# Kernel optimization log

Measured on AMD Instinct MI355X. Metric: run time of the kernel, lower is better.

The kernel has to match this reference:

```python
import jax, jax.numpy as jnp
import numpy as np

DIM = 2048
N_HEADS = 16
N_KV_HEADS = 4
HEAD_DIM = 128
SLIDING_WINDOW = 1024
ROPE_BASE = 10000.0


def _rotate_half(x):
    d = x.shape[-1] // 2
    return jnp.concatenate((-x[..., d:], x[..., :d]), axis=-1)


def _rope_cos_sin(T, dtype):
    inv_freq = 1.0 / (ROPE_BASE ** (jnp.arange(0, HEAD_DIM, 2, dtype=jnp.float32) / HEAD_DIM))
    t = jnp.arange(T, dtype=jnp.float32)
    freqs = jnp.outer(t, inv_freq)            # [T, HEAD_DIM//2]
    emb = jnp.concatenate((freqs, freqs), axis=-1)  # [T, HEAD_DIM]
    return jnp.cos(emb).astype(dtype), jnp.sin(emb).astype(dtype)


def setup_inputs() -> dict:
    key = jax.random.key(0)
    kx, kq, kk, kv, ko = jax.random.split(key, 5)
    s_in = 1.0 / np.sqrt(DIM)
    s_o = 1.0 / np.sqrt(N_HEADS * HEAD_DIM)
    return {
        "x": jax.random.normal(kx, (1, 4096, DIM), dtype=jnp.float32),
        "Wq": jax.random.normal(kq, (DIM, N_HEADS * HEAD_DIM), dtype=jnp.float32) * s_in,
        "Wk": jax.random.normal(kk, (DIM, N_KV_HEADS * HEAD_DIM), dtype=jnp.float32) * s_in,
        "Wv": jax.random.normal(kv, (DIM, N_KV_HEADS * HEAD_DIM), dtype=jnp.float32) * s_in,
        "Wo": jax.random.normal(ko, (N_HEADS * HEAD_DIM, DIM), dtype=jnp.float32) * s_o,
    }


def reference(x, Wq, Wk, Wv, Wo):
    B, T, C = x.shape
    # projections -> [B, H, T, D]
    q = (x @ Wq).reshape(B, T, N_HEADS, HEAD_DIM).transpose(0, 2, 1, 3)
    k = (x @ Wk).reshape(B, T, N_KV_HEADS, HEAD_DIM).transpose(0, 2, 1, 3)
    v = (x @ Wv).reshape(B, T, N_KV_HEADS, HEAD_DIM).transpose(0, 2, 1, 3)

    cos, sin = _rope_cos_sin(T, x.dtype)      # [T, D], broadcast over B, H
    q = q * cos + _rotate_half(q) * sin
    k = k * cos + _rotate_half(k) * sin

    # GQA: repeat kv heads (repeat_interleave over head axis)
    kv_rep = N_HEADS // N_KV_HEADS
    k = jnp.repeat(k, kv_rep, axis=1)
    v = jnp.repeat(v, kv_rep, axis=1)

    scale = 1.0 / np.sqrt(HEAD_DIM)
    att = jnp.einsum("bhqd,bhkd->bhqk", q, k) * scale  # [B, H, T, T]

    i = jnp.arange(T)[:, None]
    j = jnp.arange(T)[None, :]
    allowed = (j <= i) & ((i - j) < SLIDING_WINDOW)     # causal + sliding window
    att = jnp.where(allowed, att, -jnp.inf)
    att = jax.nn.softmax(att, axis=-1)

    y = jnp.einsum("bhqk,bhkd->bhqd", att, v)           # [B, H, T, D]
    y = y.transpose(0, 2, 1, 3).reshape(B, T, N_HEADS * HEAD_DIM)
    return y @ Wo
```

## Files before the change

kernel.cpp:

```cpp
#include <hip/hip_runtime.h>
#include <math.h>

typedef __bf16 bf16;
typedef __bf16 bf16x8 __attribute__((ext_vector_type(8)));
typedef __bf16 bf16x4 __attribute__((ext_vector_type(4)));
typedef float f32x4 __attribute__((ext_vector_type(4)));

__device__ __forceinline__ void ldg_lds16(const bf16* g, bf16* l) {
#if __has_builtin(__builtin_amdgcn_global_load_lds)
    __builtin_amdgcn_global_load_lds(
        (const __attribute__((address_space(1))) void*)g,
        (__attribute__((address_space(3))) void*)l, 16, 0, 0);
#else
    *(bf16x8*)l = *(const bf16x8*)g;
#endif
}

__global__ void cvt_x(const float* __restrict__ X, bf16* __restrict__ Xb, int total8)
{
    int idx = blockIdx.x * 256 + threadIdx.x;
    if (idx >= total8) return;
    const float* p = X + (size_t)idx * 8;
    f32x4 a = *reinterpret_cast<const f32x4*>(p);
    f32x4 b = *reinterpret_cast<const f32x4*>(p + 4);
    bf16x8 r;
    r[0] = (bf16)a[0]; r[1] = (bf16)a[1]; r[2] = (bf16)a[2]; r[3] = (bf16)a[3];
    r[4] = (bf16)b[0]; r[5] = (bf16)b[1]; r[6] = (bf16)b[2]; r[7] = (bf16)b[3];
    *reinterpret_cast<bf16x8*>(Xb + (size_t)idx * 8) = r;
}

__global__ void cvt_wt3(const float* __restrict__ Wq, const float* __restrict__ Wk,
                        const float* __restrict__ Wv, bf16* __restrict__ Wt)
{
    __shared__ float t[32][33];
    int bx = blockIdx.x;
    const float* W; int Ncols, nbase;
    if (bx < 64)      { W = Wq; Ncols = 2048; nbase = 0;    }
    else if (bx < 80) { W = Wk; Ncols = 512;  nbase = 2048; bx -= 64; }
    else              { W = Wv; Ncols = 512;  nbase = 2560; bx -= 80; }
    const int n0 = bx * 32, k0 = blockIdx.y * 32;
    const int x = threadIdx.x, y = threadIdx.y;
    #pragma unroll
    for (int i = 0; i < 4; ++i)
        t[y + 8 * i][x] = W[(size_t)(k0 + y + 8 * i) * Ncols + n0 + x];
    __syncthreads();
    #pragma unroll
    for (int i = 0; i < 4; ++i)
        Wt[(size_t)(nbase + n0 + y + 8 * i) * 2048 + k0 + x] = (bf16)t[x][y + 8 * i];
}

__global__ void cvt_wt(const float* __restrict__ W, bf16* __restrict__ Wt, int Ncols)
{
    __shared__ float t[32][33];
    const int n0 = blockIdx.x * 32, k0 = blockIdx.y * 32;
    const int x = threadIdx.x, y = threadIdx.y;
    #pragma unroll
    for (int i = 0; i < 4; ++i)
        t[y + 8 * i][x] = W[(size_t)(k0 + y + 8 * i) * Ncols + n0 + x];
    __syncthreads();
    #pragma unroll
    for (int i = 0; i < 4; ++i)
        Wt[(size_t)(n0 + y + 8 * i) * 2048 + k0 + x] = (bf16)t[x][y + 8 * i];
}

__global__ __launch_bounds__(512, 2) void gemm256_qkv(
    const bf16* __restrict__ A, const bf16* __restrict__ Bt,
    bf16* __restrict__ Qo, bf16* __restrict__ Ko, bf16* __restrict__ Vt,
    int K)
{
    __shared__ __align__(16) bf16 smem[2 * 32768];

    const int tid  = threadIdx.x;
    const int lane = tid & 63;
    const int wave = tid >> 6;
    const int quad = lane >> 4;
    const int l16  = lane & 15;
    const int wm   = wave >> 2;
    const int wn   = wave & 3;

    const int m0 = blockIdx.y * 256;
    const int n0 = blockIdx.x * 256;

    int offA[4], offB[4];
    #pragma unroll
    for (int p = 0; p < 4; ++p) {
        int u = p * 512 + tid;
        int row = u >> 3;
        int kc8 = (u & 7) ^ (row & 7);
        offA[p] = (m0 + row) * K + kc8 * 8;
        offB[p] = (n0 + row) * K + kc8 * 8;
    }
    const int dstoff = tid * 8;

    const int xv = (l16 & 7) << 4;
    const int c0 = ((quad * 16) ^ xv) >> 1;
    const int c1 = ((64 + quad * 16) ^ xv) >> 1;
    const int rA = (wm * 128 + l16) * 64;
    const int rB = (wn * 64 + l16) * 64;

    f32x4 acc[8][4] = {};
    const int NT = K >> 6;

    {
        bf16* d0 = smem;
        bf16* d1 = smem + 32768;
        #pragma unroll
        for (int p = 0; p < 4; ++p) {
            ldg_lds16(A  + offA[p], d0 + p * 4096 + dstoff);
            ldg_lds16(Bt + offB[p], d0 + 16384 + p * 4096 + dstoff);
        }
        #pragma unroll
        for (int p = 0; p < 4; ++p) {
            ldg_lds16(A  + offA[p] + 64, d1 + p * 4096 + dstoff);
            ldg_lds16(Bt + offB[p] + 64, d1 + 16384 + p * 4096 + dstoff);
        }
    }
    asm volatile("s_waitcnt vmcnt(8)" ::: "memory");
    __builtin_amdgcn_sched_barrier(0);
    __builtin_amdgcn_s_barrier();
    __builtin_amdgcn_sched_barrier(0);

    for (int t = 0; t < NT; ++t) {
        const bf16* As = smem + (t & 1) * 32768;
        const bf16* Bs = As + 16384;

        bf16x8 a0[8], b0[4];
        #pragma unroll
        for (int i = 0; i < 8; ++i)
            a0[i] = *(const bf16x8*)(As + rA + i * 1024 + c0);
        #pragma unroll
        for (int i = 0; i < 4; ++i)
            b0[i] = *(const bf16x8*)(Bs + rB + i * 1024 + c0);

        #pragma unroll
        for (int mi = 0; mi < 8; ++mi)
            #pragma unroll
            for (int ni = 0; ni < 4; ++ni)
                acc[mi][ni] = __builtin_amdgcn_mfma_f32_16x16x32_bf16(
                    a0[mi], b0[ni], acc[mi][ni], 0, 0, 0);

        bf16x8 a1[8], b1[4];
        #pragma unroll
        for (int i = 0; i < 8; ++i)
            a1[i] = *(const bf16x8*)(As + rA + i * 1024 + c1);
        #pragma unroll
        for (int i = 0; i < 4; ++i)
            b1[i] = *(const bf16x8*)(Bs + rB + i * 1024 + c1);

        asm volatile("s_waitcnt lgkmcnt(0)" ::: "memory");
        __builtin_amdgcn_sched_barrier(0);
        __builtin_amdgcn_s_barrier();
        __builtin_amdgcn_sched_barrier(0);

        if (t + 2 < NT) {
            bf16* d = smem + (t & 1) * 32768;
            const int koff = (t + 2) * 64;
            #pragma unroll
            for (int p = 0; p < 4; ++p) {
                ldg_lds16(A  + offA[p] + koff, d + p * 4096 + dstoff);
                ldg_lds16(Bt + offB[p] + koff, d + 16384 + p * 4096 + dstoff);
            }
        }

        __builtin_amdgcn_s_setprio(1);
        #pragma unroll
        for (int mi = 0; mi < 8; ++mi)
            #pragma unroll
            for (int ni = 0; ni < 4; ++ni)
                acc[mi][ni] = __builtin_amdgcn_mfma_f32_16x16x32_bf16(
                    a1[mi], b1[ni], acc[mi][ni], 0, 0, 0);
        __builtin_amdgcn_s_setprio(0);

        if (t + 2 < NT) {
            asm volatile("s_waitcnt vmcnt(8)" ::: "memory");
            __builtin_amdgcn_sched_barrier(0);
            __builtin_amdgcn_s_barrier();
            __builtin_amdgcn_sched_barrier(0);
        } else if (t == NT - 2) {
            asm volatile("s_waitcnt vmcnt(0)" ::: "memory");
            __builtin_amdgcn_sched_barrier(0);
            __builtin_amdgcn_s_barrier();
            __builtin_amdgcn_sched_barrier(0);
        }
    }

    #pragma unroll
    for (int mi = 0; mi < 8; ++mi) {
        #pragma unroll
        for (int ni = 0; ni < 4; ++ni) {
            const int row = m0 + wm * 128 + mi * 16 + quad * 4;
            const int col = n0 + wn * 64 + ni * 16 + l16;
            if (n0 < 2048) {
                #pragma unroll
                for (int r = 0; r < 4; ++r)
                    Qo[(size_t)(row + r) * 2048 + col] = (bf16)acc[mi][ni][r];
            } else if (n0 < 2560) {
                #pragma unroll
                for (int r = 0; r < 4; ++r)
                    Ko[(size_t)(row + r) * 512 + (col - 2048)] = (bf16)acc[mi][ni][r];
            } else {
                bf16x4 v;
                #pragma unroll
                for (int r = 0; r < 4; ++r) v[r] = (bf16)acc[mi][ni][r];
                *reinterpret_cast<bf16x4*>(&Vt[(size_t)(col - 2560) * 4096 + row]) = v;
            }
        }
    }
}

__global__ __launch_bounds__(512, 2) void gemm_out(
    const bf16* __restrict__ A, const bf16* __restrict__ Bt,
    float* __restrict__ C, int K)
{
    __shared__ __align__(16) bf16 smem[2 * 24576];

    const int tid  = threadIdx.x;
    const int lane = tid & 63;
    const int wave = tid >> 6;
    const int quad = lane >> 4;
    const int l16  = lane & 15;
    const int wm   = wave >> 1;
    const int wn   = wave & 1;

    const int m0 = blockIdx.y * 256;
    const int n0 = blockIdx.x * 128;

    int offA[4], offB[2];
    #pragma unroll
    for (int p = 0; p < 4; ++p) {
        int u = p * 512 + tid;
        int row = u >> 3;
        int kc8 = (u & 7) ^ (row & 7);
        offA[p] = (m0 + row) * K + kc8 * 8;
    }
    #pragma unroll
    for (int p = 0; p < 2; ++p) {
        int u = p * 512 + tid;
        int row = u >> 3;
        int kc8 = (u & 7) ^ (row & 7);
        offB[p] = (n0 + row) * K + kc8 * 8;
    }
    const int dstoff = tid * 8;

    const int xv = (l16 & 7) << 4;
    const int c0 = ((quad * 16) ^ xv) >> 1;
    const int c1 = ((64 + quad * 16) ^ xv) >> 1;
    const int rA = (wm * 64 + l16) * 64;
    const int rB = (wn * 64 + l16) * 64;

    f32x4 acc[4][4] = {};
    const int NT = K >> 6;

    auto stage = [&](int tt, int bsel) {
        bf16* as = smem + bsel * 24576;
        bf16* bs = as + 16384;
        const int koff = tt * 64;
        #pragma unroll
        for (int p = 0; p < 4; ++p)
            ldg_lds16(A + offA[p] + koff, as + p * 4096 + dstoff);
        #pragma unroll
        for (int p = 0; p < 2; ++p)
            ldg_lds16(Bt + offB[p] + koff, bs + p * 4096 + dstoff);
    };

    stage(0, 0);
    stage(1, 1);
    asm volatile("s_waitcnt vmcnt(6)" ::: "memory");
    __builtin_amdgcn_sched_barrier(0);
    __builtin_amdgcn_s_barrier();
    __builtin_amdgcn_sched_barrier(0);

    for (int t = 0; t < NT; ++t) {
        const bf16* As = smem + (t & 1) * 24576;
        const bf16* Bs = As + 16384;

        bf16x8 a0[4], b0[4];
        #pragma unroll
        for (int i = 0; i < 4; ++i)
            a0[i] = *(const bf16x8*)(As + rA + i * 1024 + c0);
        #pragma unroll
        for (int i = 0; i < 4; ++i)
            b0[i] = *(const bf16x8*)(Bs + rB + i * 1024 + c0);

        #pragma unroll
        for (int mi = 0; mi < 4; ++mi)
            #pragma unroll
            for (int ni = 0; ni < 4; ++ni)
                acc[mi][ni] = __builtin_amdgcn_mfma_f32_16x16x32_bf16(
                    a0[mi], b0[ni], acc[mi][ni], 0, 0, 0);

        bf16x8 a1[4], b1[4];
        #pragma unroll
        for (int i = 0; i < 4; ++i)
            a1[i] = *(const bf16x8*)(As + rA + i * 1024 + c1);
        #pragma unroll
        for (int i = 0; i < 4; ++i)
            b1[i] = *(const bf16x8*)(Bs + rB + i * 1024 + c1);

        asm volatile("s_waitcnt lgkmcnt(0)" ::: "memory");
        __builtin_amdgcn_sched_barrier(0);
        __builtin_amdgcn_s_barrier();
        __builtin_amdgcn_sched_barrier(0);

        if (t + 2 < NT) stage(t + 2, t & 1);

        __builtin_amdgcn_s_setprio(1);
        #pragma unroll
        for (int mi = 0; mi < 4; ++mi)
            #pragma unroll
            for (int ni = 0; ni < 4; ++ni)
                acc[mi][ni] = __builtin_amdgcn_mfma_f32_16x16x32_bf16(
                    a1[mi], b1[ni], acc[mi][ni], 0, 0, 0);
        __builtin_amdgcn_s_setprio(0);

        if (t + 2 < NT) {
            asm volatile("s_waitcnt vmcnt(6)" ::: "memory");
            __builtin_amdgcn_sched_barrier(0);
            __builtin_amdgcn_s_barrier();
            __builtin_amdgcn_sched_barrier(0);
        } else if (t == NT - 2) {
            asm volatile("s_waitcnt vmcnt(0)" ::: "memory");
            __builtin_amdgcn_sched_barrier(0);
            __builtin_amdgcn_s_barrier();
            __builtin_amdgcn_sched_barrier(0);
        }
    }

    #pragma unroll
    for (int mi = 0; mi < 4; ++mi) {
        #pragma unroll
        for (int ni = 0; ni < 4; ++ni) {
            const int row = m0 + wm * 64 + mi * 16 + quad * 4;
            const int col = n0 + wn * 64 + ni * 16 + l16;
            #pragma unroll
            for (int r = 0; r < 4; ++r)
                C[(size_t)(row + r) * 2048 + col] = acc[mi][ni][r];
        }
    }
}

__global__ void rope2_kernel(bf16* __restrict__ Qb, bf16* __restrict__ Kb,
                             int qtot, int ktot)
{
    int idx = blockIdx.x * 256 + threadIdx.x;
    bf16* base; int logH;
    if (idx < qtot) { base = Qb; logH = 4; }
    else {
        idx -= qtot;
        if (idx >= ktot) return;
        base = Kb; logH = 2;
    }
    int j  = idx & 63;
    int th = idx >> 6;
    int t  = th >> logH;

    bf16* p = base + (size_t)th * 128;
    const float NEG_LN1E4_64 = -0.14391155806323211f;
    float inv_freq = expf(NEG_LN1E4_64 * (float)j);
    float ang = (float)t * inv_freq;
    float c = cosf(ang), s = sinf(ang);
    float q0 = (float)p[j], q1 = (float)p[j + 64];
    p[j]      = (bf16)(q0 * c - q1 * s);
    p[j + 64] = (bf16)(q1 * c + q0 * s);
}

__global__ __launch_bounds__(256) void attn_v7(
    const bf16* __restrict__ Q, const bf16* __restrict__ K,
    const bf16* __restrict__ Vt, bf16* __restrict__ Y)
{
    const float scale = 0.08838834764831845f;

    __shared__ __align__(16) bf16 Ks[2 * 64 * 128];
    __shared__ __align__(16) bf16 Vs[2 * 128 * 64];
    __shared__ __align__(16) bf16 Pl[4][16 * 72];

    const int tid  = threadIdx.x;
    const int lane = tid & 63;
    const int wave = tid >> 6;
    const int quad = lane >> 4;
    const int l16  = lane & 15;

    const int i0  = (gridDim.x - 1 - blockIdx.x) * 64;
    const int h   = blockIdx.y;
    const int kvh = h >> 2;
    const int q0  = i0 + wave * 16;
    bf16* Plw = Pl[wave];

    bf16x8 qf[4];
    {
        const bf16* qp = Q + (size_t)(q0 + l16) * 2048 + h * 128 + quad * 8;
        #pragma unroll
        for (int c = 0; c < 4; ++c)
            qf[c] = *reinterpret_cast<const bf16x8*>(qp + c * 32);
    }

    f32x4 o[8] = {};
    float lsum[4] = {0.f, 0.f, 0.f, 0.f};

    const int ks = (i0 >= 1024) ? (i0 - 1024) : 0;
    const int nsteps = (i0 + 64 - ks) >> 6;

    auto stage = [&](int tt, int bsel) {
        const int k0s = ks + tt * 64;
        bf16* kd = Ks + bsel * 8192;
        bf16* vd = Vs + bsel * 8192;
        #pragma unroll
        for (int p = 0; p < 4; ++p) {
            int u = p * 256 + tid;
            int kk = u >> 4, sc = u & 15;
            ldg_lds16(K + (size_t)(k0s + kk) * 512 + kvh * 128 + (sc ^ (kk & 15)) * 8,
                      kd + u * 8);
        }
        #pragma unroll
        for (int p = 0; p < 4; ++p) {
            int u = p * 256 + tid;
            int d = u >> 3, sc = u & 7;
            ldg_lds16(Vt + (size_t)(kvh * 128 + d) * 4096 + k0s + (sc ^ (d & 7)) * 8,
                      vd + u * 8);
        }
    };

    stage(0, 0);
    stage(1, 1);
    asm volatile("s_waitcnt vmcnt(8)" ::: "memory");
    __builtin_amdgcn_sched_barrier(0);
    __builtin_amdgcn_s_barrier();
    __builtin_amdgcn_sched_barrier(0);

    for (int t = 0; t < nsteps; ++t) {
        const int b  = t & 1;
        const int k0 = ks + t * 64;
        const bf16* Kb = Ks + b * 8192;
        const bf16* Vb = Vs + b * 8192;

        f32x4 s[4];
        __builtin_amdgcn_s_setprio(1);
        #pragma unroll
        for (int kh = 0; kh < 4; ++kh) {
            const int kk = kh * 16 + l16;
            f32x4 sv = {};
            #pragma unroll
            for (int c = 0; c < 4; ++c) {
                bf16x8 kf = *reinterpret_cast<const bf16x8*>(
                    &Kb[kk * 128 + (((c * 4 + quad) ^ (kk & 15)) * 8)]);
                sv = __builtin_amdgcn_mfma_f32_16x16x32_bf16(qf[c], kf, sv, 0, 0, 0);
            }
            s[kh] = sv;
        }
        __builtin_amdgcn_s_setprio(0);

        #pragma unroll
        for (int kh = 0; kh < 4; ++kh) {
            const int key = k0 + kh * 16 + l16;
            #pragma unroll
            for (int r = 0; r < 4; ++r) {
                const int qrow = q0 + quad * 4 + r;
                bool ok = (unsigned)(qrow - key) < 1024u;
                float pv = ok ? __expf(s[kh][r] * scale) : 0.f;
                lsum[r] += pv;
                Plw[(quad * 4 + r) * 72 + kh * 16 + l16] = (bf16)pv;
            }
        }

        bf16x8 pf0 = *reinterpret_cast<const bf16x8*>(&Plw[l16 * 72 + quad * 8]);
        bf16x8 pf1 = *reinterpret_cast<const bf16x8*>(&Plw[l16 * 72 + 32 + quad * 8]);
        __builtin_amdgcn_s_setprio(1);
        #pragma unroll
        for (int n = 0; n < 8; ++n) {
            const int d = n * 16 + l16;
            bf16x8 v0 = *reinterpret_cast<const bf16x8*>(
                &Vb[d * 64 + (((quad) ^ (d & 7)) * 8)]);
            bf16x8 v1 = *reinterpret_cast<const bf16x8*>(
                &Vb[d * 64 + (((4 + quad) ^ (d & 7)) * 8)]);
            o[n] = __builtin_amdgcn_mfma_f32_16x16x32_bf16(pf0, v0, o[n], 0, 0, 0);
            o[n] = __builtin_amdgcn_mfma_f32_16x16x32_bf16(pf1, v1, o[n], 0, 0, 0);
        }
        __builtin_amdgcn_s_setprio(0);

        asm volatile("s_waitcnt lgkmcnt(0)" ::: "memory");
        __builtin_amdgcn_sched_barrier(0);
        __builtin_amdgcn_s_barrier();
        __builtin_amdgcn_sched_barrier(0);

        if (t + 2 < nsteps) {
            stage(t + 2, b);
            asm volatile("s_waitcnt vmcnt(8)" ::: "memory");
        } else {
            asm volatile("s_waitcnt vmcnt(0)" ::: "memory");
        }
        __builtin_amdgcn_sched_barrier(0);
        __builtin_amdgcn_s_barrier();
        __builtin_amdgcn_sched_barrier(0);
    }

    #pragma unroll
    for (int r = 0; r < 4; ++r) {
        #pragma unroll
        for (int off = 1; off < 16; off <<= 1)
            lsum[r] += __shfl_xor(lsum[r], off, 64);
    }
    #pragma unroll
    for (int r = 0; r < 4; ++r) {
        int row = q0 + quad * 4 + r;
        float inv = (lsum[r] > 0.f) ? 1.f / lsum[r] : 0.f;
        #pragma unroll
        for (int n = 0; n < 8; ++n)
            Y[(size_t)row * 2048 + h * 128 + n * 16 + l16] = (bf16)(o[n][r] * inv);
    }
}

extern "C" void kernel_launch(void* const* d_in, const int* in_sizes, int n_in,
                              void* d_out, int out_size, void* d_ws, size_t ws_size,
                              hipStream_t stream)
{
    const float* x  = (const float*)d_in[0];
    const float* Wq = (const float*)d_in[1];
    const float* Wk = (const float*)d_in[2];
    const float* Wv = (const float*)d_in[3];
    const float* Wo = (const float*)d_in[4];
    float* out = (float*)d_out;

    const int T = 4096, DIM = 2048;

    char* po = (char*)d_out;
    bf16* Qb = (bf16*)(po);
    bf16* Kb = (bf16*)(po + (16u << 20));
    bf16* Vtb = (bf16*)(po + (20u << 20));

    char* ws = (char*)d_ws;
    bf16* xb    = (bf16*)(ws);
    bf16* Wqkvt = (bf16*)(ws + (16u << 20));
    bf16* Yb    = (bf16*)(ws);
    bf16* Wot   = (bf16*)(ws + (16u << 20));

    cvt_x<<<dim3(T * DIM / 8 / 256), 256, 0, stream>>>(x, xb, T * DIM / 8);

    dim3 tb(32, 8);
    cvt_wt3<<<dim3(96, 64), tb, 0, stream>>>(Wq, Wk, Wv, Wqkvt);

    gemm256_qkv<<<dim3(3072 / 256, T / 256), 512, 0, stream>>>(
        xb, Wqkvt, Qb, Kb, Vtb, DIM);

    cvt_wt<<<dim3(2048 / 32, 64), tb, 0, stream>>>(Wo, Wot, 2048);

    int qtot = T * 16 * 64, ktot = T * 4 * 64;
    rope2_kernel<<<(qtot + ktot + 255) / 256, 256, 0, stream>>>(Qb, Kb, qtot, ktot);

    attn_v7<<<dim3(T / 64, 16), 256, 0, stream>>>(Qb, Kb, Vtb, Yb);

    gemm_out<<<dim3(2048 / 128, T / 256), 512, 0, stream>>>(
        Yb, Wot, out, DIM);
}
```

Measured before the change: 297.2 us.

## Fuse Q RoPE into attention and stage K/V through registers

The separate RoPE pass over Q is removed. Queries are now rotated in registers right after loading inside the attention kernel, and only K keeps a standalone RoPE kernel. The LDS double buffer fed by direct global-to-LDS loads is replaced by a single LDS buffer filled from register prefetch, which halves LDS use so more blocks may fit per CU, at the cost of extra VGPRs and a store step from registers to LDS. The P scratch tile also switches from padded rows to an XOR swizzle.

```diff
diff --git a/kernel.cpp b/kernel.cpp
--- a/kernel.cpp
+++ b/kernel.cpp
@@ -339,22 +339,15 @@
     }
 }
 
-__global__ void rope2_kernel(bf16* __restrict__ Qb, bf16* __restrict__ Kb,
-                             int qtot, int ktot)
+__global__ void rope_k(bf16* __restrict__ Kb, int total)
 {
     int idx = blockIdx.x * 256 + threadIdx.x;
-    bf16* base; int logH;
-    if (idx < qtot) { base = Qb; logH = 4; }
-    else {
-        idx -= qtot;
-        if (idx >= ktot) return;
-        base = Kb; logH = 2;
-    }
+    if (idx >= total) return;
     int j  = idx & 63;
     int th = idx >> 6;
-    int t  = th >> logH;
-
-    bf16* p = base + (size_t)th * 128;
+    int t  = th >> 2;
+
+    bf16* p = Kb + (size_t)th * 128;
     const float NEG_LN1E4_64 = -0.14391155806323211f;
     float inv_freq = expf(NEG_LN1E4_64 * (float)j);
     float ang = (float)t * inv_freq;
@@ -364,15 +357,15 @@
     p[j + 64] = (bf16)(q1 * c + q0 * s);
 }
 
-__global__ __launch_bounds__(256) void attn_v7(
+__global__ __launch_bounds__(256) void attn_v8(
     const bf16* __restrict__ Q, const bf16* __restrict__ K,
     const bf16* __restrict__ Vt, bf16* __restrict__ Y)
 {
     const float scale = 0.08838834764831845f;
 
-    __shared__ __align__(16) bf16 Ks[2 * 64 * 128];
-    __shared__ __align__(16) bf16 Vs[2 * 128 * 64];
-    __shared__ __align__(16) bf16 Pl[4][16 * 72];
+    __shared__ __align__(16) bf16 Ks[64 * 128];
+    __shared__ __align__(16) bf16 Vs[128 * 64];
+    __shared__ __align__(16) bf16 Pl[4][16 * 64];
 
     const int tid  = threadIdx.x;
     const int lane = tid & 63;
@@ -386,52 +379,75 @@
     const int q0  = i0 + wave * 16;
     bf16* Plw = Pl[wave];
 
+    const int ks = (i0 >= 1024) ? (i0 - 1024) : 0;
+    const int nsteps = (i0 + 64 - ks) >> 6;
+
+    size_t koffc[4], voffc[4];
+    #pragma unroll
+    for (int p = 0; p < 4; ++p) {
+        int u = p * 256 + tid;
+        int kk = u >> 4, sck = u & 15;
+        koffc[p] = (size_t)kk * 512 + kvh * 128 + (sck ^ (kk & 15)) * 8;
+        int d = u >> 3, scv = u & 7;
+        voffc[p] = (size_t)(kvh * 128 + d) * 4096 + (scv ^ (d & 7)) * 8;
+    }
+
+    bf16x8 kr[4], vr[4];
+    auto load_tile = [&](int tt) {
+        const int k0s = ks + tt * 64;
+        #pragma unroll
+        for (int p = 0; p < 4; ++p)
+            kr[p] = *(const bf16x8*)(K + (size_t)k0s * 512 + koffc[p]);
+        #pragma unroll
+        for (int p = 0; p < 4; ++p)
+            vr[p] = *(const bf16x8*)(Vt + (size_t)k0s + voffc[p]);
+    };
+    auto write_tile = [&]() {
+        #pragma unroll
+        for (int p = 0; p < 4; ++p)
+            *(bf16x8*)(Ks + (p * 256 + tid) * 8) = kr[p];
+        #pragma unroll
+        for (int p = 0; p < 4; ++p)
+            *(bf16x8*)(Vs + (p * 256 + tid) * 8) = vr[p];
+    };
+
+    load_tile(0);
+
     bf16x8 qf[4];
     {
         const bf16* qp = Q + (size_t)(q0 + l16) * 2048 + h * 128 + quad * 8;
+        bf16x8 qr_[4];
         #pragma unroll
         for (int c = 0; c < 4; ++c)
-            qf[c] = *reinterpret_cast<const bf16x8*>(qp + c * 32);
+            qr_[c] = *reinterpret_cast<const bf16x8*>(qp + c * 32);
+        const float NEG_LN1E4_64 = -0.14391155806323211f;
+        const float tf = (float)(q0 + l16);
+        #pragma unroll
+        for (int c = 0; c < 2; ++c) {
+            #pragma unroll
+            for (int i = 0; i < 8; ++i) {
+                float inv_freq = expf(NEG_LN1E4_64 * (float)(c * 32 + quad * 8 + i));
+                float ang = tf * inv_freq;
+                float cs = cosf(ang), sn = sinf(ang);
+                float a = (float)qr_[c][i], b = (float)qr_[c + 2][i];
+                qf[c][i]     = (bf16)(a * cs - b * sn);
+                qf[c + 2][i] = (bf16)(b * cs + a * sn);
+            }
+        }
     }
 
     f32x4 o[8] = {};
     float lsum[4] = {0.f, 0.f, 0.f, 0.f};
 
-    const int ks = (i0 >= 1024) ? (i0 - 1024) : 0;
-    const int nsteps = (i0 + 64 - ks) >> 6;
-
-    auto stage = [&](int tt, int bsel) {
-        const int k0s = ks + tt * 64;
-        bf16* kd = Ks + bsel * 8192;
-        bf16* vd = Vs + bsel * 8192;
-        #pragma unroll
-        for (int p = 0; p < 4; ++p) {
-            int u = p * 256 + tid;
-            int kk = u >> 4, sc = u & 15;
-            ldg_lds16(K + (size_t)(k0s + kk) * 512 + kvh * 128 + (sc ^ (kk & 15)) * 8,
-                      kd + u * 8);
-        }
-        #pragma unroll
-        for (int p = 0; p < 4; ++p) {
-            int u = p * 256 + tid;
-            int d = u >> 3, sc = u & 7;
-            ldg_lds16(Vt + (size_t)(kvh * 128 + d) * 4096 + k0s + (sc ^ (d & 7)) * 8,
-                      vd + u * 8);
-        }
-    };
-
-    stage(0, 0);
-    stage(1, 1);
-    asm volatile("s_waitcnt vmcnt(8)" ::: "memory");
+    write_tile();
+    load_tile(1);
+    asm volatile("s_waitcnt lgkmcnt(0)" ::: "memory");
     __builtin_amdgcn_sched_barrier(0);
     __builtin_amdgcn_s_barrier();
     __builtin_amdgcn_sched_barrier(0);
 
     for (int t = 0; t < nsteps; ++t) {
-        const int b  = t & 1;
         const int k0 = ks + t * 64;
-        const bf16* Kb = Ks + b * 8192;
-        const bf16* Vb = Vs + b * 8192;
 
         f32x4 s[4];
         __builtin_amdgcn_s_setprio(1);
@@ -442,7 +458,7 @@
             #pragma unroll
             for (int c = 0; c < 4; ++c) {
                 bf16x8 kf = *reinterpret_cast<const bf16x8*>(
-                    &Kb[kk * 128 + (((c * 4 + quad) ^ (kk & 15)) * 8)]);
+                    &Ks[kk * 128 + (((c * 4 + quad) ^ (kk & 15)) * 8)]);
                 sv = __builtin_amdgcn_mfma_f32_16x16x32_bf16(qf[c], kf, sv, 0, 0, 0);
             }
             s[kh] = sv;
@@ -458,36 +474,38 @@
                 bool ok = (unsigned)(qrow - key) < 1024u;
                 float pv = ok ? __expf(s[kh][r] * scale) : 0.f;
                 lsum[r] += pv;
-                Plw[(quad * 4 + r) * 72 + kh * 16 + l16] = (bf16)pv;
+                const int row = quad * 4 + r;
+                const int idx = row * 64 +
+                    ((((kh * 2 + (l16 >> 3)) ^ (row & 7)) << 3) | (l16 & 7));
+                Plw[idx] = (bf16)pv;
             }
         }
 
-        bf16x8 pf0 = *reinterpret_cast<const bf16x8*>(&Plw[l16 * 72 + quad * 8]);
-        bf16x8 pf1 = *reinterpret_cast<const bf16x8*>(&Plw[l16 * 72 + 32 + quad * 8]);
+        bf16x8 pf0 = *reinterpret_cast<const bf16x8*>(
+            &Plw[l16 * 64 + ((quad ^ (l16 & 7)) << 3)]);
+        bf16x8 pf1 = *reinterpret_cast<const bf16x8*>(
+            &Plw[l16 * 64 + (((4 + quad) ^ (l16 & 7)) << 3)]);
         __builtin_amdgcn_s_setprio(1);
         #pragma unroll
         for (int n = 0; n < 8; ++n) {
             const int d = n * 16 + l16;
             bf16x8 v0 = *reinterpret_cast<const bf16x8*>(
-                &Vb[d * 64 + (((quad) ^ (d & 7)) * 8)]);
+                &Vs[d * 64 + (((quad) ^ (d & 7)) * 8)]);
             bf16x8 v1 = *reinterpret_cast<const bf16x8*>(
-                &Vb[d * 64 + (((4 + quad) ^ (d & 7)) * 8)]);
+                &Vs[d * 64 + (((4 + quad) ^ (d & 7)) * 8)]);
             o[n] = __builtin_amdgcn_mfma_f32_16x16x32_bf16(pf0, v0, o[n], 0, 0, 0);
             o[n] = __builtin_amdgcn_mfma_f32_16x16x32_bf16(pf1, v1, o[n], 0, 0, 0);
         }
         __builtin_amdgcn_s_setprio(0);
 
+        __builtin_amdgcn_sched_barrier(0);
+        __builtin_amdgcn_s_barrier();
+        __builtin_amdgcn_sched_barrier(0);
+
+        if (t + 1 < nsteps) write_tile();
+        if (t + 2 < nsteps) load_tile(t + 2);
+
         asm volatile("s_waitcnt lgkmcnt(0)" ::: "memory");
-        __builtin_amdgcn_sched_barrier(0);
-        __builtin_amdgcn_s_barrier();
-        __builtin_amdgcn_sched_barrier(0);
-
-        if (t + 2 < nsteps) {
-            stage(t + 2, b);
-            asm volatile("s_waitcnt vmcnt(8)" ::: "memory");
-        } else {
-            asm volatile("s_waitcnt vmcnt(0)" ::: "memory");
-        }
         __builtin_amdgcn_sched_barrier(0);
         __builtin_amdgcn_s_barrier();
         __builtin_amdgcn_sched_barrier(0);
@@ -543,10 +561,10 @@
 
     cvt_wt<<<dim3(2048 / 32, 64), tb, 0, stream>>>(Wo, Wot, 2048);
 
-    int qtot = T * 16 * 64, ktot = T * 4 * 64;
-    rope2_kernel<<<(qtot + ktot + 255) / 256, 256, 0, stream>>>(Qb, Kb, qtot, ktot);
-
-    attn_v7<<<dim3(T / 64, 16), 256, 0, stream>>>(Qb, Kb, Vtb, Yb);
+    int ktot = T * 4 * 64;
+    rope_k<<<(ktot + 255) / 256, 256, 0, stream>>>(Kb, ktot);
+
+    attn_v8<<<dim3(T / 64, 16), 256, 0, stream>>>(Qb, Kb, Vtb, Yb);
 
     gemm_out<<<dim3(2048 / 128, T / 256), 512, 0, stream>>>(
         Yb, Wot, out, DIM);
```

Result: no change. 295.3 us (-0.7%).

## Fuse Q RoPE into attention, skip masking on full tiles, swizzle P buffer

Applied to the files above, without the earlier changes.

The separate rope kernel now rotates only K. Q RoPE is applied in registers inside the attention kernel after Q is loaded, which removes a global read and write pass over Q. Fully unmasked key tiles take a fast path with no mask test. The per-wave P staging buffer drops its 72-element padding in favour of an XOR swizzle to avoid bank conflicts. The trade-off is extra transcendental math per attention block, since each block recomputes RoPE angles for its Q rows.

```diff
diff --git a/kernel.cpp b/kernel.cpp
--- a/kernel.cpp
+++ b/kernel.cpp
@@ -339,22 +339,15 @@
     }
 }
 
-__global__ void rope2_kernel(bf16* __restrict__ Qb, bf16* __restrict__ Kb,
-                             int qtot, int ktot)
+__global__ void rope_k(bf16* __restrict__ Kb, int total)
 {
     int idx = blockIdx.x * 256 + threadIdx.x;
-    bf16* base; int logH;
-    if (idx < qtot) { base = Qb; logH = 4; }
-    else {
-        idx -= qtot;
-        if (idx >= ktot) return;
-        base = Kb; logH = 2;
-    }
+    if (idx >= total) return;
     int j  = idx & 63;
     int th = idx >> 6;
-    int t  = th >> logH;
-
-    bf16* p = base + (size_t)th * 128;
+    int t  = th >> 2;
+
+    bf16* p = Kb + (size_t)th * 128;
     const float NEG_LN1E4_64 = -0.14391155806323211f;
     float inv_freq = expf(NEG_LN1E4_64 * (float)j);
     float ang = (float)t * inv_freq;
@@ -364,7 +357,7 @@
     p[j + 64] = (bf16)(q1 * c + q0 * s);
 }
 
-__global__ __launch_bounds__(256) void attn_v7(
+__global__ __launch_bounds__(256) void attn_v9(
     const bf16* __restrict__ Q, const bf16* __restrict__ K,
     const bf16* __restrict__ Vt, bf16* __restrict__ Y)
 {
@@ -372,7 +365,7 @@
 
     __shared__ __align__(16) bf16 Ks[2 * 64 * 128];
     __shared__ __align__(16) bf16 Vs[2 * 128 * 64];
-    __shared__ __align__(16) bf16 Pl[4][16 * 72];
+    __shared__ __align__(16) bf16 Pl[4][16 * 64];
 
     const int tid  = threadIdx.x;
     const int lane = tid & 63;
@@ -386,17 +379,6 @@
     const int q0  = i0 + wave * 16;
     bf16* Plw = Pl[wave];
 
-    bf16x8 qf[4];
-    {
-        const bf16* qp = Q + (size_t)(q0 + l16) * 2048 + h * 128 + quad * 8;
-        #pragma unroll
-        for (int c = 0; c < 4; ++c)
-            qf[c] = *reinterpret_cast<const bf16x8*>(qp + c * 32);
-    }
-
-    f32x4 o[8] = {};
-    float lsum[4] = {0.f, 0.f, 0.f, 0.f};
-
     const int ks = (i0 >= 1024) ? (i0 - 1024) : 0;
     const int nsteps = (i0 + 64 - ks) >> 6;
 
@@ -422,6 +404,33 @@
 
     stage(0, 0);
     stage(1, 1);
+
+    bf16x8 qf[4];
+    {
+        const bf16* qp = Q + (size_t)(q0 + l16) * 2048 + h * 128 + quad * 8;
+        bf16x8 qr_[4];
+        #pragma unroll
+        for (int c = 0; c < 4; ++c)
+            qr_[c] = *reinterpret_cast<const bf16x8*>(qp + c * 32);
+        const float NEG_LN1E4_64 = -0.14391155806323211f;
+        const float tf = (float)(q0 + l16);
+        #pragma unroll
+        for (int c = 0; c < 2; ++c) {
+            #pragma unroll
+            for (int i = 0; i < 8; ++i) {
+                float inv_freq = expf(NEG_LN1E4_64 * (float)(c * 32 + quad * 8 + i));
+                float ang = tf * inv_freq;
+                float cs = cosf(ang), sn = sinf(ang);
+                float a = (float)qr_[c][i], b = (float)qr_[c + 2][i];
+                qf[c][i]     = (bf16)(a * cs - b * sn);
+                qf[c + 2][i] = (bf16)(b * cs + a * sn);
+            }
+        }
+    }
+
+    f32x4 o[8] = {};
+    float lsum[4] = {0.f, 0.f, 0.f, 0.f};
+
     asm volatile("s_waitcnt vmcnt(8)" ::: "memory");
     __builtin_amdgcn_sched_barrier(0);
     __builtin_amdgcn_s_barrier();
@@ -449,21 +458,42 @@
         }
         __builtin_amdgcn_s_setprio(0);
 
-        #pragma unroll
-        for (int kh = 0; kh < 4; ++kh) {
-            const int key = k0 + kh * 16 + l16;
-            #pragma unroll
-            for (int r = 0; r < 4; ++r) {
-                const int qrow = q0 + quad * 4 + r;
-                bool ok = (unsigned)(qrow - key) < 1024u;
-                float pv = ok ? __expf(s[kh][r] * scale) : 0.f;
-                lsum[r] += pv;
-                Plw[(quad * 4 + r) * 72 + kh * 16 + l16] = (bf16)pv;
+        const bool full = (k0 + 63 <= q0) && (q0 + 15 - k0 < 1024);
+        if (full) {
+            #pragma unroll
+            for (int kh = 0; kh < 4; ++kh) {
+                #pragma unroll
+                for (int r = 0; r < 4; ++r) {
+                    float pv = __expf(s[kh][r] * scale);
+                    lsum[r] += pv;
+                    const int row = quad * 4 + r;
+                    const int idx = row * 64 +
+                        ((((kh * 2 + (l16 >> 3)) ^ (row & 7)) << 3) | (l16 & 7));
+                    Plw[idx] = (bf16)pv;
+                }
             }
-        }
-
-        bf16x8 pf0 = *reinterpret_cast<const bf16x8*>(&Plw[l16 * 72 + quad * 8]);
-        bf16x8 pf1 = *reinterpret_cast<const bf16x8*>(&Plw[l16 * 72 + 32 + quad * 8]);
+        } else {
+            #pragma unroll
+            for (int kh = 0; kh < 4; ++kh) {
+                const int key = k0 + kh * 16 + l16;
+                #pragma unroll
+                for (int r = 0; r < 4; ++r) {
+                    const int qrow = q0 + quad * 4 + r;
+                    bool ok = (unsigned)(qrow - key) < 1024u;
+                    float pv = ok ? __expf(s[kh][r] * scale) : 0.f;
+                    lsum[r] += pv;
+                    const int row = quad * 4 + r;
+                    const int idx = row * 64 +
+                        ((((kh * 2 + (l16 >> 3)) ^ (row & 7)) << 3) | (l16 & 7));
+                    Plw[idx] = (bf16)pv;
+                }
+            }
+        }
+
+        bf16x8 pf0 = *reinterpret_cast<const bf16x8*>(
+            &Plw[l16 * 64 + ((quad ^ (l16 & 7)) << 3)]);
+        bf16x8 pf1 = *reinterpret_cast<const bf16x8*>(
+            &Plw[l16 * 64 + (((4 + quad) ^ (l16 & 7)) << 3)]);
         __builtin_amdgcn_s_setprio(1);
         #pragma unroll
         for (int n = 0; n < 8; ++n) {
@@ -543,10 +573,10 @@
 
     cvt_wt<<<dim3(2048 / 32, 64), tb, 0, stream>>>(Wo, Wot, 2048);
 
-    int qtot = T * 16 * 64, ktot = T * 4 * 64;
-    rope2_kernel<<<(qtot + ktot + 255) / 256, 256, 0, stream>>>(Qb, Kb, qtot, ktot);
-
-    attn_v7<<<dim3(T / 64, 16), 256, 0, stream>>>(Qb, Kb, Vtb, Yb);
+    int ktot = T * 4 * 64;
+    rope_k<<<(ktot + 255) / 256, 256, 0, stream>>>(Kb, ktot);
+
+    attn_v9<<<dim3(T / 64, 16), 256, 0, stream>>>(Qb, Kb, Vtb, Yb);
 
     gemm_out<<<dim3(2048 / 128, T / 256), 512, 0, stream>>>(
         Yb, Wot, out, DIM);
```

Result: faster. 289.1 us (-2.7%).
